# Optimization experiments

Hardware: AMD Instinct MI355X
Metric: run time of the kernel (lower is better)

The kernel has to match this reference:

```python
import jax, jax.numpy as jnp
import numpy as np


def setup_inputs() -> dict:
    key = jax.random.key(0)
    k0, k1, k2, k3 = jax.random.split(key, 4)
    B, S, D, F, E = 2, 2048, 1024, 4096, 8
    hidden_states = jax.random.normal(k0, (B, S, D), dtype=jnp.float32)
    Wr = jax.random.normal(k1, (E, D), dtype=jnp.float32) * 0.02   # router Linear weight [E, D]
    W1 = jax.random.normal(k2, (E, D, F), dtype=jnp.float32) * 0.02  # expert w1 (transposed torch layout)
    W2 = jax.random.normal(k3, (E, F, D), dtype=jnp.float32) * 0.02  # expert w2
    return {"hidden_states": hidden_states, "Wr": Wr, "W1": W1, "W2": W2, "top_k": 2}


def reference(hidden_states, Wr, W1, W2, top_k):
    # hidden_states: [B, S, D]; Wr: [E, D]; W1: [E, D, F]; W2: [E, F, D]
    E = Wr.shape[0]
    dt = hidden_states.dtype

    # Router: logits -> top-k expert indices. NOTE: the original module computes
    # softmax routing weights over the top-k logits but never applies them in the
    # combine step, so the output is an UNWEIGHTED sum over selected experts.
    router_logits = jnp.einsum('bsd,ed->bse', hidden_states, Wr)
    _, topk_idx = jax.lax.top_k(router_logits, top_k)            # [B, S, K]

    # mask[b,s,e] = 1 if expert e is in token (b,s)'s top-k (indices are distinct)
    mask = (jax.nn.one_hot(topk_idx, E, dtype=dt).sum(axis=-2) > 0).astype(dt)  # [B, S, E]

    # Dense per-expert FFN (SiLU MLP, no bias, dropout=identity in eval):
    h = jax.nn.silu(jnp.einsum('bsd,edf->bsef', hidden_states, W1))  # [B, S, E, F]
    y = jnp.einsum('bsef,efd->bsed', h, W2)                          # [B, S, E, D]

    # Combine: unweighted sum over selected experts (faithful to source)
    return jnp.einsum('bsed,bse->bsd', y, mask)
```

## Files before the change

### kernel.cpp

```cpp
#include <hip/hip_runtime.h>
#include <hip/hip_bf16.h>
#include <stdint.h>

#define TOKENS 4096
#define DDIM 1024
#define FDIM 4096
#define NEXP 8
#define BM 128
#define BN 128
#define BK2 32

typedef __attribute__((ext_vector_type(4))) float f32x4;
typedef __attribute__((ext_vector_type(8))) short short8;

__device__ __forceinline__ unsigned short f2bf(float f) {
    union { float f; uint32_t u; } v; v.f = f;
    uint32_t u = v.u;
    return (unsigned short)((u + 0x7fff + ((u >> 16) & 1)) >> 16);
}

#define BARRIER() asm volatile("s_barrier" ::: "memory")
#define WAIT_VM0() asm volatile("s_waitcnt vmcnt(0)" ::: "memory")
#define WAIT_VM4() asm volatile("s_waitcnt vmcnt(4)" ::: "memory")
#define WAIT_VM8() asm volatile("s_waitcnt vmcnt(8)" ::: "memory")
#define GLDS(SRC, DST) __builtin_amdgcn_global_load_lds( \
    (const __attribute__((address_space(1))) void*)(SRC), \
    (__attribute__((address_space(3))) void*)(DST), 16, 0, 0)

__global__ __launch_bounds__(256) void cvt_x(const float* __restrict__ x,
                                             unsigned short* __restrict__ xb, int n) {
    int i = (blockIdx.x * 256 + threadIdx.x) * 8;
    if (i >= n) return;
    float4 a = *(const float4*)(x + i);
    float4 b = *(const float4*)(x + i + 4);
    short8 o;
    o[0] = f2bf(a.x); o[1] = f2bf(a.y); o[2] = f2bf(a.z); o[3] = f2bf(a.w);
    o[4] = f2bf(b.x); o[5] = f2bf(b.y); o[6] = f2bf(b.z); o[7] = f2bf(b.w);
    *(short8*)(xb + i) = o;
}

__global__ __launch_bounds__(256) void transpose_cvt(const float* __restrict__ in,
                                                     unsigned short* __restrict__ out,
                                                     int R, int C) {
    __shared__ float tile[32][33];
    int e = blockIdx.z;
    int r0 = blockIdx.y * 32, c0 = blockIdx.x * 32;
    const float* src = in + (size_t)e * R * C;
    unsigned short* dst = out + (size_t)e * R * C;
    int t = threadIdx.x;
    int rr = t >> 3;
    int cc = (t & 7) * 4;
    float4 v = *(const float4*)(src + (size_t)(r0 + rr) * C + c0 + cc);
    tile[rr][cc + 0] = v.x; tile[rr][cc + 1] = v.y;
    tile[rr][cc + 2] = v.z; tile[rr][cc + 3] = v.w;
    __syncthreads();
    int oc = rr;
    int orr = cc;
    ushort4 o;
    o.x = f2bf(tile[orr + 0][oc]);
    o.y = f2bf(tile[orr + 1][oc]);
    o.z = f2bf(tile[orr + 2][oc]);
    o.w = f2bf(tile[orr + 3][oc]);
    *(ushort4*)(dst + (size_t)(c0 + oc) * R + r0 + orr) = o;
}

__global__ __launch_bounds__(256) void router(const float* __restrict__ x,
                                              const float* __restrict__ wr,
                                              int* __restrict__ cnt,
                                              int* __restrict__ list) {
    __shared__ float wl[NEXP * DDIM];
    int t = threadIdx.x;
    for (int i = t; i < NEXP * DDIM; i += 256) wl[i] = wr[i];
    __syncthreads();
    int tok = blockIdx.x * 4 + (t >> 6);
    int lane = t & 63;
    float acc[NEXP];
#pragma unroll
    for (int e = 0; e < NEXP; e++) acc[e] = 0.f;
    const float* xr = x + (size_t)tok * DDIM;
    for (int d = lane; d < DDIM; d += 64) {
        float xv = xr[d];
#pragma unroll
        for (int e = 0; e < NEXP; e++) acc[e] += xv * wl[e * DDIM + d];
    }
#pragma unroll
    for (int e = 0; e < NEXP; e++) {
#pragma unroll
        for (int off = 32; off; off >>= 1) acc[e] += __shfl_xor(acc[e], off);
    }
    if (lane == 0) {
        int e1 = 0; float v1 = acc[0];
        for (int e = 1; e < NEXP; e++) if (acc[e] > v1) { v1 = acc[e]; e1 = e; }
        int e2 = -1; float v2 = -1e30f;
        for (int e = 0; e < NEXP; e++) if (e != e1 && acc[e] > v2) { v2 = acc[e]; e2 = e; }
        int p1 = atomicAdd(&cnt[e1], 1);
        list[e1 * TOKENS + p1] = tok;
        int p2 = atomicAdd(&cnt[e2], 1);
        list[e2 * TOKENS + p2] = tok;
    }
}

__global__ void setup(const int* __restrict__ cnt, int* __restrict__ off,
                      int* __restrict__ wbA, int* __restrict__ wbB,
                      int* __restrict__ qctr, int* __restrict__ tot) {
    if (threadIdx.x == 0) {
        int s = 0, ta = 0, tb = 0;
        for (int e = 0; e < NEXP; e++) {
            off[e] = s; s += cnt[e];
            wbA[e] = ta; wbB[e] = tb;
            int nt = (cnt[e] + BM - 1) / BM;
            ta += nt * (FDIM / BN);
            tb += nt * (DDIM / BN);
        }
        wbA[NEXP] = ta; wbB[NEXP] = tb;
        tot[0] = ta; tot[1] = tb;
        qctr[0] = 0; qctr[1] = 0;
    }
}

template <bool GATHER_A, bool SILU>
__global__ __launch_bounds__(256, 2) void gemm_moe4(
    const unsigned short* __restrict__ Abase,
    const unsigned short* __restrict__ Wt,
    const int* __restrict__ cnt, const int* __restrict__ off,
    const int* __restrict__ list,
    const int* __restrict__ wbase,
    int* __restrict__ qctr, const int* __restrict__ tot,
    unsigned short* __restrict__ Hout,
    float* __restrict__ Yout,
    int KD, int NDIM) {
    __shared__ alignas(16) unsigned short As[4][BM * BK2];
    __shared__ alignas(16) unsigned short Bs[4][BN * BK2];
    __shared__ int wsh;

    int t = threadIdx.x;
    int lane = t & 63;
    int wid = t >> 6;
    int wm = wid >> 1, wn = wid & 1;
    int r16 = lane & 15, g = lane >> 4;
    const int total = *tot;

#define FRAG32(TILE, ROW, G) (*(const short8*)&(TILE)[(ROW) * BK2 + ((((G) ^ (((ROW) >> 1) & 3))) << 3)])

    for (;;) {
        if (t == 0) wsh = atomicAdd(qctr, 1);
        __syncthreads();
        int w = wsh;
        if (w >= total) break;

        int e = 0;
        while (e < NEXP - 1 && w >= wbase[e + 1]) e++;
        w -= wbase[e];
        int n_e = cnt[e];
        int ntm = (n_e + BM - 1) >> 7;
        int by = w / ntm;
        int mtile = w - by * ntm;
        int m0 = mtile * BM;
        int n0 = by * BN;
        int base = off[e];

        const unsigned short* pA[2];
        const unsigned short* pB[2];
        int ldsOff[2];
#pragma unroll
        for (int i = 0; i < 2; i++) {
            int c = i * 256 + t;
            int row = c >> 2, p = c & 3;
            int cg = p ^ ((row >> 1) & 3);
            int arow = m0 + row; if (arow >= n_e) arow = n_e - 1;
            size_t grow = GATHER_A ? (size_t)list[e * TOKENS + arow] : (size_t)(base + arow);
            pA[i] = Abase + grow * (size_t)KD + (cg << 3);
            pB[i] = Wt + ((size_t)e * NDIM + n0 + row) * (size_t)KD + (cg << 3);
            ldsOff[i] = c * 16;
        }

        f32x4 acc[4][4];
#pragma unroll
        for (int i = 0; i < 4; i++)
#pragma unroll
            for (int j = 0; j < 4; j++) acc[i][j] = f32x4{0.f, 0.f, 0.f, 0.f};

#pragma unroll
        for (int s = 0; s < 3; ++s) {
#pragma unroll
            for (int i = 0; i < 2; i++) { GLDS(pA[i], (char*)As[s] + ldsOff[i]); pA[i] += BK2; }
#pragma unroll
            for (int i = 0; i < 2; i++) { GLDS(pB[i], (char*)Bs[s] + ldsOff[i]); pB[i] += BK2; }
        }
        WAIT_VM8();
        BARRIER();

        const int NT = KD / BK2;
        for (int tk = 0; tk < NT; ++tk) {
            const int rs = tk & 3;
            const unsigned short* Ac = As[rs];
            const unsigned short* Bc = Bs[rs];

            if (tk + 3 < NT) {
                const int ws_ = (tk + 3) & 3;
#pragma unroll
                for (int i = 0; i < 2; i++) { GLDS(pA[i], (char*)As[ws_] + ldsOff[i]); pA[i] += BK2; }
#pragma unroll
                for (int i = 0; i < 2; i++) { GLDS(pB[i], (char*)Bs[ws_] + ldsOff[i]); pB[i] += BK2; }
            }

            short8 a0, a1, a2, a3, b0, b1, b2, b3;
            a0 = FRAG32(Ac, wm * 64 + 0 * 16 + r16, g);
            a1 = FRAG32(Ac, wm * 64 + 1 * 16 + r16, g);
            a2 = FRAG32(Ac, wm * 64 + 2 * 16 + r16, g);
            a3 = FRAG32(Ac, wm * 64 + 3 * 16 + r16, g);
            b0 = FRAG32(Bc, wn * 64 + 0 * 16 + r16, g);
            b1 = FRAG32(Bc, wn * 64 + 1 * 16 + r16, g);
            b2 = FRAG32(Bc, wn * 64 + 2 * 16 + r16, g);
            b3 = FRAG32(Bc, wn * 64 + 3 * 16 + r16, g);
            __builtin_amdgcn_s_setprio(1);
            acc[0][0] = __builtin_amdgcn_mfma_f32_16x16x32_bf16(a0, b0, acc[0][0], 0, 0, 0);
            acc[0][1] = __builtin_amdgcn_mfma_f32_16x16x32_bf16(a0, b1, acc[0][1], 0, 0, 0);
            acc[0][2] = __builtin_amdgcn_mfma_f32_16x16x32_bf16(a0, b2, acc[0][2], 0, 0, 0);
            acc[0][3] = __builtin_amdgcn_mfma_f32_16x16x32_bf16(a0, b3, acc[0][3], 0, 0, 0);
            acc[1][0] = __builtin_amdgcn_mfma_f32_16x16x32_bf16(a1, b0, acc[1][0], 0, 0, 0);
            acc[1][1] = __builtin_amdgcn_mfma_f32_16x16x32_bf16(a1, b1, acc[1][1], 0, 0, 0);
            acc[1][2] = __builtin_amdgcn_mfma_f32_16x16x32_bf16(a1, b2, acc[1][2], 0, 0, 0);
            acc[1][3] = __builtin_amdgcn_mfma_f32_16x16x32_bf16(a1, b3, acc[1][3], 0, 0, 0);
            acc[2][0] = __builtin_amdgcn_mfma_f32_16x16x32_bf16(a2, b0, acc[2][0], 0, 0, 0);
            acc[2][1] = __builtin_amdgcn_mfma_f32_16x16x32_bf16(a2, b1, acc[2][1], 0, 0, 0);
            acc[2][2] = __builtin_amdgcn_mfma_f32_16x16x32_bf16(a2, b2, acc[2][2], 0, 0, 0);
            acc[2][3] = __builtin_amdgcn_mfma_f32_16x16x32_bf16(a2, b3, acc[2][3], 0, 0, 0);
            acc[3][0] = __builtin_amdgcn_mfma_f32_16x16x32_bf16(a3, b0, acc[3][0], 0, 0, 0);
            acc[3][1] = __builtin_amdgcn_mfma_f32_16x16x32_bf16(a3, b1, acc[3][1], 0, 0, 0);
            acc[3][2] = __builtin_amdgcn_mfma_f32_16x16x32_bf16(a3, b2, acc[3][2], 0, 0, 0);
            acc[3][3] = __builtin_amdgcn_mfma_f32_16x16x32_bf16(a3, b3, acc[3][3], 0, 0, 0);
            __builtin_amdgcn_s_setprio(0);

            if (tk + 1 < NT) {
                if (tk + 3 < NT)      WAIT_VM8();
                else if (tk + 2 < NT) WAIT_VM4();
                else                  WAIT_VM0();
                BARRIER();
            }
        }

#pragma unroll
        for (int mi = 0; mi < 4; ++mi) {
#pragma unroll
            for (int nj = 0; nj < 4; ++nj) {
#pragma unroll
                for (int qq = 0; qq < 4; ++qq) {
                    int lr = wm * 64 + mi * 16 + g * 4 + qq;
                    if (m0 + lr < n_e) {
                        int col = n0 + wn * 64 + nj * 16 + r16;
                        float v = acc[mi][nj][qq];
                        if (SILU) {
                            v = v / (1.f + __expf(-v));
                            Hout[(size_t)(base + m0 + lr) * NDIM + col] = f2bf(v);
                        } else {
                            int tok = list[e * TOKENS + m0 + lr];
                            atomicAdd(&Yout[(size_t)tok * NDIM + col], v);
                        }
                    }
                }
            }
        }
    }
#undef FRAG32
}

extern "C" void kernel_launch(void* const* d_in, const int* in_sizes, int n_in,
                              void* d_out, int out_size, void* d_ws, size_t ws_size,
                              hipStream_t stream) {
    const float* X  = (const float*)d_in[0];
    const float* Wr = (const float*)d_in[1];
    const float* W1 = (const float*)d_in[2];
    const float* W2 = (const float*)d_in[3];
    float* Y = (float*)d_out;

    char* ws = (char*)d_ws;
    int* cnt  = (int*)(ws + 0);
    int* off  = (int*)(ws + 64);
    int* wbA  = (int*)(ws + 128);
    int* wbB  = (int*)(ws + 192);
    int* qctr = (int*)(ws + 256);
    int* tot  = (int*)(ws + 288);
    int* list = (int*)(ws + 1024);
    unsigned short* Xb = (unsigned short*)(ws + (1ull << 20));
    unsigned short* WT = (unsigned short*)(ws + (16ull << 20));
    unsigned short* H  = (unsigned short*)(ws + (80ull << 20));

    hipMemsetAsync(d_out, 0, (size_t)out_size * sizeof(float), stream);
    hipMemsetAsync(cnt, 0, 32, stream);

    cvt_x<<<TOKENS * DDIM / (256 * 8), 256, 0, stream>>>(X, Xb, TOKENS * DDIM);
    router<<<TOKENS / 4, 256, 0, stream>>>(X, Wr, cnt, list);
    setup<<<1, 64, 0, stream>>>(cnt, off, wbA, wbB, qctr, tot);

    transpose_cvt<<<dim3(FDIM / 32, DDIM / 32, NEXP), 256, 0, stream>>>(W1, WT, DDIM, FDIM);
    gemm_moe4<true, true><<<512, 256, 0, stream>>>(
        Xb, WT, cnt, off, list, wbA, qctr + 0, tot + 0, H, nullptr, DDIM, FDIM);

    transpose_cvt<<<dim3(DDIM / 32, FDIM / 32, NEXP), 256, 0, stream>>>(W2, WT, FDIM, DDIM);
    gemm_moe4<false, false><<<512, 256, 0, stream>>>(
        H, WT, cnt, off, list, wbB, qctr + 1, tot + 1, nullptr, Y, FDIM, DDIM);
}
```

Before: 555.2 us.

## Use per-XCD work queues, double-buffered LDS, and higher occupancy in MoE GEMMs

Replaces the single global atomic work counter with eight contiguous work ranges, one per XCD. Each block picks its range from the hardware XCC_ID register and steals from neighbouring ranges once its own is empty. This aims to keep tiles that share weight panels on the same XCD's L2 and to cut contention on one atomic. The 4-stage LDS pipeline becomes a 2-stage double buffer with a full vmcnt(0) wait each iteration. In exchange, launch bounds rise to 4 blocks per CU and the grid doubles to 1024 blocks, giving more latency hiding through occupancy at the cost of shallower prefetch.

```diff
diff --git a/kernel.cpp b/kernel.cpp
--- a/kernel.cpp
+++ b/kernel.cpp
@@ -21,8 +21,6 @@
 
 #define BARRIER() asm volatile("s_barrier" ::: "memory")
 #define WAIT_VM0() asm volatile("s_waitcnt vmcnt(0)" ::: "memory")
-#define WAIT_VM4() asm volatile("s_waitcnt vmcnt(4)" ::: "memory")
-#define WAIT_VM8() asm volatile("s_waitcnt vmcnt(8)" ::: "memory")
 #define GLDS(SRC, DST) __builtin_amdgcn_global_load_lds( \
     (const __attribute__((address_space(1))) void*)(SRC), \
     (__attribute__((address_space(3))) void*)(DST), 16, 0, 0)
@@ -102,7 +100,8 @@
 
 __global__ void setup(const int* __restrict__ cnt, int* __restrict__ off,
                       int* __restrict__ wbA, int* __restrict__ wbB,
-                      int* __restrict__ qctr, int* __restrict__ tot) {
+                      int* __restrict__ qA, int* __restrict__ qlA,
+                      int* __restrict__ qB, int* __restrict__ qlB) {
     if (threadIdx.x == 0) {
         int s = 0, ta = 0, tb = 0;
         for (int e = 0; e < NEXP; e++) {
@@ -113,24 +112,28 @@
             tb += nt * (DDIM / BN);
         }
         wbA[NEXP] = ta; wbB[NEXP] = tb;
-        tot[0] = ta; tot[1] = tb;
-        qctr[0] = 0; qctr[1] = 0;
+        for (int x = 0; x < 8; x++) {
+            qA[x]  = (int)((long)ta * x / 8);
+            qlA[x] = (int)((long)ta * (x + 1) / 8);
+            qB[x]  = (int)((long)tb * x / 8);
+            qlB[x] = (int)((long)tb * (x + 1) / 8);
+        }
     }
 }
 
 template <bool GATHER_A, bool SILU>
-__global__ __launch_bounds__(256, 2) void gemm_moe4(
+__global__ __launch_bounds__(256, 4) void gemm_moe6(
     const unsigned short* __restrict__ Abase,
     const unsigned short* __restrict__ Wt,
     const int* __restrict__ cnt, const int* __restrict__ off,
     const int* __restrict__ list,
     const int* __restrict__ wbase,
-    int* __restrict__ qctr, const int* __restrict__ tot,
+    int* __restrict__ qctr, const int* __restrict__ qlim,
     unsigned short* __restrict__ Hout,
     float* __restrict__ Yout,
     int KD, int NDIM) {
-    __shared__ alignas(16) unsigned short As[4][BM * BK2];
-    __shared__ alignas(16) unsigned short Bs[4][BN * BK2];
+    __shared__ alignas(16) unsigned short As[2][BM * BK2];
+    __shared__ alignas(16) unsigned short Bs[2][BN * BK2];
     __shared__ int wsh;
 
     int t = threadIdx.x;
@@ -138,15 +141,27 @@
     int wid = t >> 6;
     int wm = wid >> 1, wn = wid & 1;
     int r16 = lane & 15, g = lane >> 4;
-    const int total = *tot;
+
+    uint32_t xcd;
+    asm volatile("s_getreg_b32 %0, hwreg(HW_REG_XCC_ID)" : "=s"(xcd));
+    int myq = (int)(xcd & 7);
+    int tries = 0;
 
 #define FRAG32(TILE, ROW, G) (*(const short8*)&(TILE)[(ROW) * BK2 + ((((G) ^ (((ROW) >> 1) & 3))) << 3)])
 
     for (;;) {
-        if (t == 0) wsh = atomicAdd(qctr, 1);
+        if (t == 0) {
+            int w = -1;
+            while (tries < 8) {
+                w = atomicAdd(&qctr[myq], 1);
+                if (w < qlim[myq]) break;
+                myq = (myq + 1) & 7; ++tries; w = -1;
+            }
+            wsh = w;
+        }
         __syncthreads();
         int w = wsh;
-        if (w >= total) break;
+        if (w < 0) break;
 
         int e = 0;
         while (e < NEXP - 1 && w >= wbase[e + 1]) e++;
@@ -181,38 +196,36 @@
             for (int j = 0; j < 4; j++) acc[i][j] = f32x4{0.f, 0.f, 0.f, 0.f};
 
 #pragma unroll
-        for (int s = 0; s < 3; ++s) {
-#pragma unroll
-            for (int i = 0; i < 2; i++) { GLDS(pA[i], (char*)As[s] + ldsOff[i]); pA[i] += BK2; }
-#pragma unroll
-            for (int i = 0; i < 2; i++) { GLDS(pB[i], (char*)Bs[s] + ldsOff[i]); pB[i] += BK2; }
-        }
-        WAIT_VM8();
+        for (int i = 0; i < 2; i++) { GLDS(pA[i], (char*)As[0] + ldsOff[i]); pA[i] += BK2; }
+#pragma unroll
+        for (int i = 0; i < 2; i++) { GLDS(pB[i], (char*)Bs[0] + ldsOff[i]); pB[i] += BK2; }
+        WAIT_VM0();
         BARRIER();
 
         const int NT = KD / BK2;
         for (int tk = 0; tk < NT; ++tk) {
-            const int rs = tk & 3;
-            const unsigned short* Ac = As[rs];
-            const unsigned short* Bc = Bs[rs];
-
-            if (tk + 3 < NT) {
-                const int ws_ = (tk + 3) & 3;
-#pragma unroll
-                for (int i = 0; i < 2; i++) { GLDS(pA[i], (char*)As[ws_] + ldsOff[i]); pA[i] += BK2; }
-#pragma unroll
-                for (int i = 0; i < 2; i++) { GLDS(pB[i], (char*)Bs[ws_] + ldsOff[i]); pB[i] += BK2; }
+            const int cur = tk & 1;
+            const unsigned short* Ac = As[cur];
+            const unsigned short* Bc = Bs[cur];
+
+            short8 a0 = FRAG32(Ac, wm * 64 + 0 * 16 + r16, g);
+            short8 a1 = FRAG32(Ac, wm * 64 + 1 * 16 + r16, g);
+            short8 a2 = FRAG32(Ac, wm * 64 + 2 * 16 + r16, g);
+            short8 a3 = FRAG32(Ac, wm * 64 + 3 * 16 + r16, g);
+            short8 b0 = FRAG32(Bc, wn * 64 + 0 * 16 + r16, g);
+            short8 b1 = FRAG32(Bc, wn * 64 + 1 * 16 + r16, g);
+            short8 b2 = FRAG32(Bc, wn * 64 + 2 * 16 + r16, g);
+            short8 b3 = FRAG32(Bc, wn * 64 + 3 * 16 + r16, g);
+
+            if (tk + 1 < NT) {
+                char* Ad = (char*)As[cur ^ 1];
+                char* Bd = (char*)Bs[cur ^ 1];
+#pragma unroll
+                for (int i = 0; i < 2; i++) { GLDS(pA[i], Ad + ldsOff[i]); pA[i] += BK2; }
+#pragma unroll
+                for (int i = 0; i < 2; i++) { GLDS(pB[i], Bd + ldsOff[i]); pB[i] += BK2; }
             }
 
-            short8 a0, a1, a2, a3, b0, b1, b2, b3;
-            a0 = FRAG32(Ac, wm * 64 + 0 * 16 + r16, g);
-            a1 = FRAG32(Ac, wm * 64 + 1 * 16 + r16, g);
-            a2 = FRAG32(Ac, wm * 64 + 2 * 16 + r16, g);
-            a3 = FRAG32(Ac, wm * 64 + 3 * 16 + r16, g);
-            b0 = FRAG32(Bc, wn * 64 + 0 * 16 + r16, g);
-            b1 = FRAG32(Bc, wn * 64 + 1 * 16 + r16, g);
-            b2 = FRAG32(Bc, wn * 64 + 2 * 16 + r16, g);
-            b3 = FRAG32(Bc, wn * 64 + 3 * 16 + r16, g);
             __builtin_amdgcn_s_setprio(1);
             acc[0][0] = __builtin_amdgcn_mfma_f32_16x16x32_bf16(a0, b0, acc[0][0], 0, 0, 0);
             acc[0][1] = __builtin_amdgcn_mfma_f32_16x16x32_bf16(a0, b1, acc[0][1], 0, 0, 0);
@@ -232,12 +245,8 @@
             acc[3][3] = __builtin_amdgcn_mfma_f32_16x16x32_bf16(a3, b3, acc[3][3], 0, 0, 0);
             __builtin_amdgcn_s_setprio(0);
 
-            if (tk + 1 < NT) {
-                if (tk + 3 < NT)      WAIT_VM8();
-                else if (tk + 2 < NT) WAIT_VM4();
-                else                  WAIT_VM0();
-                BARRIER();
-            }
+            WAIT_VM0();
+            BARRIER();
         }
 
 #pragma unroll
@@ -279,8 +288,10 @@
     int* off  = (int*)(ws + 64);
     int* wbA  = (int*)(ws + 128);
     int* wbB  = (int*)(ws + 192);
-    int* qctr = (int*)(ws + 256);
-    int* tot  = (int*)(ws + 288);
+    int* qA   = (int*)(ws + 256);
+    int* qlA  = (int*)(ws + 288);
+    int* qB   = (int*)(ws + 320);
+    int* qlB  = (int*)(ws + 352);
     int* list = (int*)(ws + 1024);
     unsigned short* Xb = (unsigned short*)(ws + (1ull << 20));
     unsigned short* WT = (unsigned short*)(ws + (16ull << 20));
@@ -291,13 +302,13 @@
 
     cvt_x<<<TOKENS * DDIM / (256 * 8), 256, 0, stream>>>(X, Xb, TOKENS * DDIM);
     router<<<TOKENS / 4, 256, 0, stream>>>(X, Wr, cnt, list);
-    setup<<<1, 64, 0, stream>>>(cnt, off, wbA, wbB, qctr, tot);
+    setup<<<1, 64, 0, stream>>>(cnt, off, wbA, wbB, qA, qlA, qB, qlB);
 
     transpose_cvt<<<dim3(FDIM / 32, DDIM / 32, NEXP), 256, 0, stream>>>(W1, WT, DDIM, FDIM);
-    gemm_moe4<true, true><<<512, 256, 0, stream>>>(
-        Xb, WT, cnt, off, list, wbA, qctr + 0, tot + 0, H, nullptr, DDIM, FDIM);
+    gemm_moe6<true, true><<<1024, 256, 0, stream>>>(
+        Xb, WT, cnt, off, list, wbA, qA, qlA, H, nullptr, DDIM, FDIM);
 
     transpose_cvt<<<dim3(DDIM / 32, FDIM / 32, NEXP), 256, 0, stream>>>(W2, WT, FDIM, DDIM);
-    gemm_moe4<false, false><<<512, 256, 0, stream>>>(
-        H, WT, cnt, off, list, wbB, qctr + 1, tot + 1, nullptr, Y, FDIM, DDIM);
-}
+    gemm_moe6<false, false><<<1024, 256, 0, stream>>>(
+        H, WT, cnt, off, list, wbB, qB, qlB, nullptr, Y, FDIM, DDIM);
+}
```

New measurement: 1.412 ms. 154% more time.
